# Performance work log

Hardware: AMD Instinct MI355X
Metric: run time of the kernel (lower is better)

## Reference

```python
import jax, jax.numpy as jnp
import numpy as np

DIM = 2048
STATE = 16
BATCH = 2
SEQ = 2048
LN_EPS = 1e-5


def setup_inputs() -> dict:
    key = jax.random.key(0)
    ks = jax.random.split(key, 12)
    d, n = DIM, STATE
    inp = {
        "x": jax.random.normal(ks[0], (BATCH, SEQ, d), dtype=jnp.float32),
        "ln_gamma": jnp.ones((d,), dtype=jnp.float32),
        "ln_beta": jnp.zeros((d,), dtype=jnp.float32),
        # proj_in: Linear(d, 2d) (spectral-normed; weights treated as effective)
        "W_in": jax.random.normal(ks[1], (2 * d, d), dtype=jnp.float32) / np.sqrt(d),
        "b_in": jnp.zeros((2 * d,), dtype=jnp.float32),
        "state_A": jax.random.normal(ks[2], (n, d), dtype=jnp.float32) * 0.01,
        "W_B": jax.random.normal(ks[3], (n, d), dtype=jnp.float32) / np.sqrt(d),
        "b_B": jnp.zeros((n,), dtype=jnp.float32),
        "W_C": jax.random.normal(ks[4], (n, d), dtype=jnp.float32) / np.sqrt(d),
        "b_C": jnp.zeros((n,), dtype=jnp.float32),
        "W_dt": jax.random.normal(ks[5], (d, d), dtype=jnp.float32) / np.sqrt(d),
        "b_dt": jnp.zeros((d,), dtype=jnp.float32),
        "W_out": jax.random.normal(ks[6], (d, d), dtype=jnp.float32) / np.sqrt(d),
        "b_out": jnp.zeros((d,), dtype=jnp.float32),
    }
    return inp


def reference(x, ln_gamma, ln_beta, W_in, b_in, state_A, W_B, b_B, W_C, b_C,
              W_dt, b_dt, W_out, b_out):
    residual = x
    # LayerNorm over last dim
    mu = jnp.mean(x, axis=-1, keepdims=True)
    var = jnp.mean(jnp.square(x - mu), axis=-1, keepdims=True)
    xn = (x - mu) * jax.lax.rsqrt(var + LN_EPS) * ln_gamma + ln_beta
    # input projection and gate split
    xz = jnp.einsum('bsd,ed->bse', xn, W_in) + b_in          # (B,S,2D)
    x_ssm, z = jnp.split(xz, 2, axis=-1)                      # (B,S,D) each
    # dt = clamp(softplus(proj_dt(x_ssm)), max=1.0)
    dt = jnp.minimum(jax.nn.softplus(jnp.einsum('bsd,ed->bse', x_ssm, W_dt) + b_dt), 1.0)
    Bm = jnp.einsum('bsd,nd->bsn', x_ssm, W_B) + b_B          # (B,S,N)
    Cm = jnp.einsum('bsd,nd->bsn', x_ssm, W_C) + b_C          # (B,S,N)
    # A_bar[b,s,n,d] = exp(state_A[n,d] * dt[b,s,d])
    A_bar = jnp.exp(state_A[None, None, :, :] * dt[:, :, None, :])  # (B,S,N,D)
    # y[b,s,d] = sum_n C[b,s,n]*B[b,s,n]*A_bar[b,s,n,d] * x_ssm[b,s,d]
    y = jnp.einsum('bsn,bsnd->bsd', Cm * Bm, A_bar) * x_ssm
    gated = y * jax.nn.silu(z)
    out = jnp.einsum('bsd,ed->bse', gated, W_out) + b_out
    return out + residual
```

## Files before the change

kernel.cpp:

```cpp
#include <hip/hip_runtime.h>

typedef unsigned short u16;
typedef float f32x4 __attribute__((ext_vector_type(4)));
typedef __bf16 bf16x8 __attribute__((ext_vector_type(8)));

__device__ __forceinline__ u16 f2bf(float f) {
    unsigned u = __float_as_uint(f);
    u += 0x7FFFu + ((u >> 16) & 1u);
    return (u16)(u >> 16);
}
__device__ __forceinline__ float b2f(u16 h) {
    return __uint_as_float(((unsigned)h) << 16);
}

__device__ __forceinline__ void async16(const u16* g, u16* l) {
    __builtin_amdgcn_global_load_lds(
        (__attribute__((address_space(1))) void*)(u16*)g,
        (__attribute__((address_space(3))) void*)l,
        16, 0, 0);
}

#define T_TOK 4096
#define DIM   2048

__global__ __launch_bounds__(256) void castln_all(const float* __restrict__ W_in,
                                                  u16* __restrict__ wb_in,
                                                  const float* __restrict__ W_dt,
                                                  u16* __restrict__ wb_dt,
                                                  const float* __restrict__ W_B,
                                                  const float* __restrict__ W_C,
                                                  const float* __restrict__ W_out,
                                                  u16* __restrict__ wb_out,
                                                  const float* __restrict__ x,
                                                  const float* __restrict__ g,
                                                  const float* __restrict__ b,
                                                  u16* __restrict__ o) {
    __shared__ float s1[4], s2[4];
    int blk = blockIdx.x, tid = threadIdx.x;
    if (blk < 16448) {
        const float* s; u16* d; int j;
        if (blk < 8192)       { s = W_in;  d = wb_in;  j = blk * 256 + tid; }
        else if (blk < 12288) { s = W_dt;  d = wb_dt;  j = (blk - 8192) * 256 + tid; }
        else if (blk < 12320) { s = W_B;   d = wb_dt + (size_t)2048 * 2048;
                                j = (blk - 12288) * 256 + tid; }
        else if (blk < 12352) { s = W_C;   d = wb_dt + (size_t)2064 * 2048;
                                j = (blk - 12320) * 256 + tid; }
        else                  { s = W_out; d = wb_out; j = (blk - 12352) * 256 + tid; }
        float4 f = ((const float4*)s)[j];
        ushort4 u;
        u.x = f2bf(f.x); u.y = f2bf(f.y); u.z = f2bf(f.z); u.w = f2bf(f.w);
        ((ushort4*)d)[j] = u;
        return;
    }
    int t = blk - 16448;
    int wave = tid >> 6, lane = tid & 63;
    size_t base = (size_t)t * DIM;
    int d0 = tid * 8;
    float4 v0 = *(const float4*)(x + base + d0);
    float4 v1 = *(const float4*)(x + base + d0 + 4);
    float v[8] = {v0.x, v0.y, v0.z, v0.w, v1.x, v1.y, v1.z, v1.w};
    float s = 0.f;
#pragma unroll
    for (int j = 0; j < 8; ++j) s += v[j];
#pragma unroll
    for (int o2 = 32; o2; o2 >>= 1) s += __shfl_xor(s, o2);
    if (lane == 0) s1[wave] = s;
    __syncthreads();
    float mu = (s1[0] + s1[1] + s1[2] + s1[3]) * (1.f / DIM);
    float q = 0.f;
#pragma unroll
    for (int j = 0; j < 8; ++j) { float dd = v[j] - mu; q += dd * dd; }
#pragma unroll
    for (int o2 = 32; o2; o2 >>= 1) q += __shfl_xor(q, o2);
    if (lane == 0) s2[wave] = q;
    __syncthreads();
    float var = (s2[0] + s2[1] + s2[2] + s2[3]) * (1.f / DIM);
    float rs = rsqrtf(var + 1e-5f);
    float4 g0 = *(const float4*)(g + d0), g1 = *(const float4*)(g + d0 + 4);
    float4 b0 = *(const float4*)(b + d0), b1 = *(const float4*)(b + d0 + 4);
    float gv[8] = {g0.x, g0.y, g0.z, g0.w, g1.x, g1.y, g1.z, g1.w};
    float bv[8] = {b0.x, b0.y, b0.z, b0.w, b1.x, b1.y, b1.z, b1.w};
    ushort4 r0, r1;
    u16* rp0 = (u16*)&r0; u16* rp1 = (u16*)&r1;
#pragma unroll
    for (int j = 0; j < 4; ++j) {
        rp0[j] = f2bf((v[j] - mu) * rs * gv[j] + bv[j]);
        rp1[j] = f2bf((v[j + 4] - mu) * rs * gv[j + 4] + bv[j + 4]);
    }
    *(ushort4*)(o + base + d0) = r0;
    *(ushort4*)(o + base + d0 + 4) = r1;
}

#define GBM 256
#define GBN 256
#define GBK 64

#define WAITV2 asm volatile("s_waitcnt vmcnt(2)" ::: "memory")

__global__ __launch_bounds__(512) void gemm_wide(const u16* __restrict__ A,
                                                 const u16* __restrict__ W,
                                                 const float* __restrict__ bias,
                                                 u16* __restrict__ Xs,
                                                 u16* __restrict__ Z, int K) {
    __shared__ __align__(16) u16 lA[2][GBM * GBK];
    __shared__ __align__(16) u16 lB[2][GBN * GBK];
    const int tid = threadIdx.x;
    const int wv = tid >> 6, lane = tid & 63;
    const int quad = lane >> 4, l16 = lane & 15;
    const int wr = wv >> 2, wc = wv & 3;
    const int tM = blockIdx.x * GBM, tN = blockIdx.y * GBN;

    const int srow = tid >> 3;
    const int swz = ((tid & 7) ^ (srow & 7)) * 8;
    const u16* gA = A + (size_t)(tM + srow) * 2048 + swz;
    const u16* gW = W + (size_t)(tN + srow) * 2048 + swz;

#define STAGE_AH(BI, KC, H) do {                                              \
    _Pragma("unroll") for (int r_ = 2 * (H); r_ < 2 * (H) + 2; ++r_)          \
      async16(gA + (size_t)r_ * 64 * 2048 + (KC),                             \
              &lA[BI][(r_ * 64 + wv * 8) * GBK]);                             \
  } while (0)
#define STAGE_BH(BI, KC, H) do {                                              \
    _Pragma("unroll") for (int r_ = 2 * (H); r_ < 2 * (H) + 2; ++r_)          \
      async16(gW + (size_t)r_ * 64 * 2048 + (KC),                             \
              &lB[BI][(r_ * 64 + wv * 8) * GBK]);                             \
  } while (0)

    int aoff[2][4][2], boff[2][2][2];
#pragma unroll
    for (int qm = 0; qm < 2; ++qm)
#pragma unroll
        for (int mi = 0; mi < 4; ++mi)
#pragma unroll
            for (int h = 0; h < 2; ++h) {
                int row = wr * 128 + (qm * 4 + mi) * 16 + l16;
                aoff[qm][mi][h] = row * GBK + (((h * 4 + quad) ^ (l16 & 7)) * 8);
            }
#pragma unroll
    for (int qn = 0; qn < 2; ++qn)
#pragma unroll
        for (int ni = 0; ni < 2; ++ni)
#pragma unroll
            for (int h = 0; h < 2; ++h) {
                int row = wc * 64 + (qn * 2 + ni) * 16 + l16;
                boff[qn][ni][h] = row * GBK + (((h * 4 + quad) ^ (l16 & 7)) * 8);
            }

    f32x4 acc[8][4] = {};
    bf16x8 af[4][2];

#define PHASE(BI, QM, QN, LOADA, STAGE_STMT, WAIT_STMT) do {                  \
    if (LOADA) {                                                              \
      _Pragma("unroll") for (int mi_ = 0; mi_ < 4; ++mi_)                     \
        _Pragma("unroll") for (int h_ = 0; h_ < 2; ++h_)                      \
          af[mi_][h_] = *(const bf16x8*)&lA[BI][aoff[QM][mi_][h_]];           \
    }                                                                         \
    bf16x8 bfr_[2][2];                                                        \
    _Pragma("unroll") for (int ni_ = 0; ni_ < 2; ++ni_)                       \
      _Pragma("unroll") for (int h_ = 0; h_ < 2; ++h_)                        \
        bfr_[ni_][h_] = *(const bf16x8*)&lB[BI][boff[QN][ni_][h_]];           \
    STAGE_STMT;                                                               \
    __builtin_amdgcn_s_setprio(1);                                            \
    _Pragma("unroll") for (int mi_ = 0; mi_ < 4; ++mi_)                       \
      _Pragma("unroll") for (int ni_ = 0; ni_ < 2; ++ni_)                     \
        _Pragma("unroll") for (int h_ = 0; h_ < 2; ++h_)                      \
          acc[QM * 4 + mi_][QN * 2 + ni_] =                                   \
              __builtin_amdgcn_mfma_f32_16x16x32_bf16(                        \
                  af[mi_][h_], bfr_[ni_][h_],                                 \
                  acc[QM * 4 + mi_][QN * 2 + ni_], 0, 0, 0);                  \
    __builtin_amdgcn_s_setprio(0);                                            \
    WAIT_STMT;                                                                \
    __builtin_amdgcn_s_barrier();                                             \
  } while (0)

    STAGE_AH(0, 0, 0);
    STAGE_AH(0, 0, 1);
    STAGE_BH(0, 0, 0);
    STAGE_BH(0, 0, 1);
    STAGE_AH(1, 64, 0);
    WAITV2;
    __builtin_amdgcn_s_barrier();

    const int NIT = K >> 7;
    for (int it = 0; it < NIT; ++it) {
        const int k1 = it * 128 + 64;
        int kn = it * 128 + 128;
        if (kn > K - 64) kn = K - 64;
        int kn1 = it * 128 + 192;
        if (kn1 > K - 64) kn1 = K - 64;

        PHASE(0, 0, 0, 1, STAGE_AH(1, k1, 1),  (void)0);
        PHASE(0, 0, 1, 0, STAGE_BH(1, k1, 0),  (void)0);
        PHASE(0, 1, 0, 1, STAGE_BH(1, k1, 1),  (void)0);
        PHASE(0, 1, 1, 0, STAGE_AH(0, kn, 0),  WAITV2);
        PHASE(1, 0, 0, 1, STAGE_AH(0, kn, 1),  (void)0);
        PHASE(1, 0, 1, 0, STAGE_BH(0, kn, 0),  (void)0);
        PHASE(1, 1, 0, 1, STAGE_BH(0, kn, 1),  (void)0);
        PHASE(1, 1, 1, 0, STAGE_AH(1, kn1, 0), WAITV2);
    }

    asm volatile("s_waitcnt vmcnt(0)" ::: "memory");

    const bool isb_z = (tN >= 2048);
    u16* dst = isb_z ? Z : Xs;
#pragma unroll
    for (int mi = 0; mi < 8; ++mi) {
#pragma unroll
        for (int ni = 0; ni < 4; ++ni) {
            int col = tN + wc * 64 + ni * 16 + l16;
            float bv = bias[col];
            int ocol = isb_z ? (col - 2048) : col;
#pragma unroll
            for (int r = 0; r < 4; ++r) {
                int row = tM + wr * 128 + mi * 16 + quad * 4 + r;
                dst[(size_t)row * 2048 + ocol] = f2bf(acc[mi][ni][r] + bv);
            }
        }
    }
#undef PHASE
#undef STAGE_AH
#undef STAGE_BH
}

#define DBM 128
#define DBN 128
#define DBK 64

template <int EPI>
__global__ __launch_bounds__(256) void gemm128(const u16* __restrict__ A,
                                               const u16* __restrict__ W,
                                               const float* __restrict__ bias,
                                               const float* __restrict__ resid,
                                               void* __restrict__ C,
                                               u16* __restrict__ dots, int K) {
    __shared__ __align__(16) u16 lAB[(DBM + DBN) * DBK];
    const int tid = threadIdx.x;
    const int wave = tid >> 6, lane = tid & 63;
    const int quad = lane >> 4, l16 = lane & 15;
    const int tM = blockIdx.x * DBM;
    const int tN = blockIdx.y * DBN;
    const int wr = wave >> 1, wc = wave & 1;

    const int rowin = tid >> 3;
    const int col8 = ((tid & 7) ^ (rowin & 7)) * 8;
    const u16* gptr[8];
    u16* ldst[8];
#pragma unroll
    for (int i = 0; i < 8; ++i) {
        int trow = i * 32 + rowin;
        const u16* src = (i < 4) ? (A + (size_t)(tM + trow) * 2048)
                                 : (W + (size_t)(tN + (trow - DBM)) * 2048);
        gptr[i] = src + col8;
        ldst[i] = &lAB[(i * 32 + wave * 8) * DBK];
    }

    int a_off[2][4], b_off[2][4];
#pragma unroll
    for (int h = 0; h < 2; ++h) {
#pragma unroll
        for (int mi = 0; mi < 4; ++mi)
            a_off[h][mi] = (wr * 64 + mi * 16 + l16) * DBK +
                           (((h * 4 + quad) ^ (l16 & 7)) * 8);
#pragma unroll
        for (int ni = 0; ni < 4; ++ni)
            b_off[h][ni] = (DBM + wc * 64 + ni * 16 + l16) * DBK +
                           (((h * 4 + quad) ^ (l16 & 7)) * 8);
    }

    f32x4 acc[4][4] = {};

    for (int kt = 0; kt < K; kt += DBK) {
#pragma unroll
        for (int i = 0; i < 8; ++i) async16(gptr[i] + kt, ldst[i]);
        __syncthreads();
#pragma unroll
        for (int h = 0; h < 2; ++h) {
            bf16x8 af[4], bfr[4];
#pragma unroll
            for (int i = 0; i < 4; ++i) af[i] = *(const bf16x8*)&lAB[a_off[h][i]];
#pragma unroll
            for (int i = 0; i < 4; ++i) bfr[i] = *(const bf16x8*)&lAB[b_off[h][i]];
#pragma unroll
            for (int mi = 0; mi < 4; ++mi)
#pragma unroll
                for (int ni = 0; ni < 4; ++ni)
                    acc[mi][ni] = __builtin_amdgcn_mfma_f32_16x16x32_bf16(
                        af[mi], bfr[ni], acc[mi][ni], 0, 0, 0);
        }
        __syncthreads();
    }

#pragma unroll
    for (int mi = 0; mi < 4; ++mi) {
#pragma unroll
        for (int ni = 0; ni < 4; ++ni) {
            int col = tN + wc * 64 + ni * 16 + l16;
#pragma unroll
            for (int r = 0; r < 4; ++r) {
                int row = tM + wr * 64 + mi * 16 + quad * 4 + r;
                if constexpr (EPI == 1) {
                    if (col < 2048) {
                        float v = acc[mi][ni][r] + bias[col];
                        float sp = (v > 0.5413f) ? 1.0f
                                                 : __logf(1.0f + __expf(v));
                        ((u16*)C)[(size_t)row * 2048 + col] = f2bf(sp);
                    } else if (col < 2080) {
                        dots[(size_t)row * 32 + (col - 2048)] =
                            f2bf(acc[mi][ni][r]);
                    }
                } else {
                    size_t idx = (size_t)row * 2048 + col;
                    ((float*)C)[idx] = acc[mi][ni][r] + bias[col] + resid[idx];
                }
            }
        }
    }
}

__global__ __launch_bounds__(256) void ssm_gate2_kernel(const u16* __restrict__ dtb,
                                                        const u16* __restrict__ xsb,
                                                        u16* __restrict__ zg,
                                                        const float* __restrict__ A,
                                                        const u16* __restrict__ dots,
                                                        const float* __restrict__ bB,
                                                        const float* __restrict__ bC) {
    __shared__ float Pl[8][16];
    const int tid = threadIdx.x;
    const int t0 = blockIdx.x * 8;
    const int d0 = tid * 8;

    float a[16][8];
#pragma unroll
    for (int n = 0; n < 16; ++n) {
        float4 a0 = *(const float4*)(A + n * DIM + d0);
        float4 a1 = *(const float4*)(A + n * DIM + d0 + 4);
        a[n][0] = a0.x; a[n][1] = a0.y; a[n][2] = a0.z; a[n][3] = a0.w;
        a[n][4] = a1.x; a[n][5] = a1.y; a[n][6] = a1.z; a[n][7] = a1.w;
    }
    if (tid < 128) {
        int tt = tid >> 4, n = tid & 15;
        float Bv = b2f(dots[(size_t)(t0 + tt) * 32 + n]) + bB[n];
        float Cv = b2f(dots[(size_t)(t0 + tt) * 32 + 16 + n]) + bC[n];
        Pl[tt][n] = Bv * Cv;
    }
    __syncthreads();

    for (int tt = 0; tt < 8; ++tt) {
        size_t dbase = (size_t)(t0 + tt) * DIM;
        ushort4 dth0 = *(const ushort4*)(dtb + dbase + d0);
        ushort4 dth1 = *(const ushort4*)(dtb + dbase + d0 + 4);
        ushort4 xsh0 = *(const ushort4*)(xsb + dbase + d0);
        ushort4 xsh1 = *(const ushort4*)(xsb + dbase + d0 + 4);
        ushort4 zh0  = *(const ushort4*)(zg + dbase + d0);
        ushort4 zh1  = *(const ushort4*)(zg + dbase + d0 + 4);
        float dtv[8], xsv[8], zv[8];
        const u16* dp0 = (const u16*)&dth0; const u16* dp1 = (const u16*)&dth1;
        const u16* xp0 = (const u16*)&xsh0; const u16* xp1 = (const u16*)&xsh1;
        const u16* zp0 = (const u16*)&zh0;  const u16* zp1 = (const u16*)&zh1;
#pragma unroll
        for (int j = 0; j < 4; ++j) {
            dtv[j] = b2f(dp0[j]); dtv[j + 4] = b2f(dp1[j]);
            xsv[j] = b2f(xp0[j]); xsv[j + 4] = b2f(xp1[j]);
            zv[j]  = b2f(zp0[j]); zv[j + 4]  = b2f(zp1[j]);
        }
        float s[8] = {};
#pragma unroll
        for (int n = 0; n < 16; ++n) {
            float pn = Pl[tt][n];
#pragma unroll
            for (int j = 0; j < 8; ++j) s[j] += pn * __expf(a[n][j] * dtv[j]);
        }
        ushort4 r0, r1;
        u16* rp0 = (u16*)&r0; u16* rp1 = (u16*)&r1;
#pragma unroll
        for (int j = 0; j < 8; ++j) {
            float y = s[j] * xsv[j];
            float sz = zv[j] * (1.0f / (1.0f + __expf(-zv[j])));
            u16 hv = f2bf(y * sz);
            if (j < 4) rp0[j] = hv; else rp1[j - 4] = hv;
        }
        *(ushort4*)(zg + dbase + d0) = r0;
        *(ushort4*)(zg + dbase + d0 + 4) = r1;
    }
}

extern "C" void kernel_launch(void* const* d_in, const int* in_sizes, int n_in,
                              void* d_out, int out_size, void* d_ws, size_t ws_size,
                              hipStream_t stream) {
    const float* x      = (const float*)d_in[0];
    const float* ln_g   = (const float*)d_in[1];
    const float* ln_b   = (const float*)d_in[2];
    const float* W_in   = (const float*)d_in[3];
    const float* b_in   = (const float*)d_in[4];
    const float* stateA = (const float*)d_in[5];
    const float* W_B    = (const float*)d_in[6];
    const float* b_B    = (const float*)d_in[7];
    const float* W_C    = (const float*)d_in[8];
    const float* b_C    = (const float*)d_in[9];
    const float* W_dt   = (const float*)d_in[10];
    const float* b_dt   = (const float*)d_in[11];
    const float* W_out  = (const float*)d_in[12];
    const float* b_out  = (const float*)d_in[13];

    char* ws = (char*)d_ws;
    u16*   wb_in  = (u16*)(ws);
    u16*   dotsb  = (u16*)(ws);
    u16*   xnb    = (u16*)(ws + 16777216);
    u16*   dtb    = (u16*)(ws + 16777216);
    u16*   xsb    = (u16*)(ws + 33554432);
    u16*   zg     = (u16*)(ws + 50331648);
    u16*   wb_dt  = (u16*)(ws + 67108864);
    u16*   wb_out = (u16*)(ws + 75759616);

    castln_all<<<20544, 256, 0, stream>>>(W_in, wb_in, W_dt, wb_dt, W_B, W_C,
                                          W_out, wb_out, x, ln_g, ln_b, xnb);
    gemm_wide<<<dim3(16, 16), 512, 0, stream>>>(xnb, wb_in, b_in, xsb, zg, 2048);
    gemm128<1><<<dim3(32, 17), 256, 0, stream>>>(xsb, wb_dt, b_dt, nullptr,
                                                 dtb, dotsb, 2048);
    ssm_gate2_kernel<<<512, 256, 0, stream>>>(dtb, xsb, zg, stateA, dotsb,
                                              b_B, b_C);
    gemm128<2><<<dim3(32, 16), 256, 0, stream>>>(zg, wb_out, b_out, x,
                                                 (float*)d_out, nullptr, 2048);
}
```

Measured before the change: 396.0 us.

## Double-buffer LDS in narrow-tile GEMMs for dt and output projections

Replaces the 128x128 single-buffered GEMM with a 128x64 tile that keeps two LDS buffers, issuing async loads for the next K-step while MFMAs run on the current one. This drops one barrier per iteration. The narrower tile doubles the grid (about 1056 and 1024 blocks) to fill more CUs on the 4096x2048 problems. The trade-off is lower arithmetic intensity per tile and more total global traffic for the A operand.

```diff
diff --git a/kernel.cpp b/kernel.cpp
--- a/kernel.cpp
+++ b/kernel.cpp
@@ -222,95 +222,107 @@
 #undef STAGE_BH
 }
 
-#define DBM 128
-#define DBN 128
-#define DBK 64
+#define NBM 128
+#define NBN 64
+#define NBK 64
 
 template <int EPI>
-__global__ __launch_bounds__(256) void gemm128(const u16* __restrict__ A,
-                                               const u16* __restrict__ W,
+__global__ __launch_bounds__(256) void gemm_nw(const u16* __restrict__ A, int lda,
+                                               const u16* __restrict__ W, int ldw,
                                                const float* __restrict__ bias,
                                                const float* __restrict__ resid,
-                                               void* __restrict__ C,
-                                               u16* __restrict__ dots, int K) {
-    __shared__ __align__(16) u16 lAB[(DBM + DBN) * DBK];
+                                               void* __restrict__ C, int ldc, int K,
+                                               u16* __restrict__ dots) {
+    __shared__ __align__(16) u16 lAB[2][(NBM + NBN) * NBK];
     const int tid = threadIdx.x;
     const int wave = tid >> 6, lane = tid & 63;
     const int quad = lane >> 4, l16 = lane & 15;
-    const int tM = blockIdx.x * DBM;
-    const int tN = blockIdx.y * DBN;
+    const int tM = blockIdx.x * NBM;
+    const int tN = blockIdx.y * NBN;
     const int wr = wave >> 1, wc = wave & 1;
 
     const int rowin = tid >> 3;
     const int col8 = ((tid & 7) ^ (rowin & 7)) * 8;
-    const u16* gptr[8];
-    u16* ldst[8];
-#pragma unroll
-    for (int i = 0; i < 8; ++i) {
+    const u16* gptr[6];
+    int loff[6];
+#pragma unroll
+    for (int i = 0; i < 6; ++i) {
         int trow = i * 32 + rowin;
-        const u16* src = (i < 4) ? (A + (size_t)(tM + trow) * 2048)
-                                 : (W + (size_t)(tN + (trow - DBM)) * 2048);
+        const u16* src = (i < 4) ? (A + (size_t)(tM + trow) * lda)
+                                 : (W + (size_t)(tN + (trow - NBM)) * ldw);
         gptr[i] = src + col8;
-        ldst[i] = &lAB[(i * 32 + wave * 8) * DBK];
-    }
-
-    int a_off[2][4], b_off[2][4];
+        loff[i] = (i * 32 + wave * 8) * NBK;
+    }
+
+    int a_off[2][4], b_off[2][2];
 #pragma unroll
     for (int h = 0; h < 2; ++h) {
 #pragma unroll
         for (int mi = 0; mi < 4; ++mi)
-            a_off[h][mi] = (wr * 64 + mi * 16 + l16) * DBK +
+            a_off[h][mi] = (wr * 64 + mi * 16 + l16) * NBK +
                            (((h * 4 + quad) ^ (l16 & 7)) * 8);
 #pragma unroll
-        for (int ni = 0; ni < 4; ++ni)
-            b_off[h][ni] = (DBM + wc * 64 + ni * 16 + l16) * DBK +
+        for (int ni = 0; ni < 2; ++ni)
+            b_off[h][ni] = (NBM + wc * 32 + ni * 16 + l16) * NBK +
                            (((h * 4 + quad) ^ (l16 & 7)) * 8);
     }
 
-    f32x4 acc[4][4] = {};
-
-    for (int kt = 0; kt < K; kt += DBK) {
-#pragma unroll
-        for (int i = 0; i < 8; ++i) async16(gptr[i] + kt, ldst[i]);
+    f32x4 acc[4][2] = {};
+
+#define STAGE_NW(BUF, KT) do {                                                \
+    _Pragma("unroll") for (int i_ = 0; i_ < 6; ++i_)                          \
+      async16(gptr[i_] + (KT), &lAB[BUF][loff[i_]]);                          \
+  } while (0)
+
+    STAGE_NW(0, 0);
+    __syncthreads();
+
+    int cur = 0;
+    for (int kt = 0; kt < K; kt += NBK) {
+        if (kt + NBK < K) STAGE_NW(cur ^ 1, kt + NBK);
+        const u16* Lb = lAB[cur];
+        bf16x8 af[2][4], bfr[2][2];
+#pragma unroll
+        for (int h = 0; h < 2; ++h) {
+#pragma unroll
+            for (int mi = 0; mi < 4; ++mi) af[h][mi] = *(const bf16x8*)&Lb[a_off[h][mi]];
+#pragma unroll
+            for (int ni = 0; ni < 2; ++ni) bfr[h][ni] = *(const bf16x8*)&Lb[b_off[h][ni]];
+        }
+#pragma unroll
+        for (int h = 0; h < 2; ++h)
+#pragma unroll
+            for (int mi = 0; mi < 4; ++mi)
+#pragma unroll
+                for (int ni = 0; ni < 2; ++ni)
+                    acc[mi][ni] = __builtin_amdgcn_mfma_f32_16x16x32_bf16(
+                        af[h][mi], bfr[h][ni], acc[mi][ni], 0, 0, 0);
         __syncthreads();
-#pragma unroll
-        for (int h = 0; h < 2; ++h) {
-            bf16x8 af[4], bfr[4];
-#pragma unroll
-            for (int i = 0; i < 4; ++i) af[i] = *(const bf16x8*)&lAB[a_off[h][i]];
-#pragma unroll
-            for (int i = 0; i < 4; ++i) bfr[i] = *(const bf16x8*)&lAB[b_off[h][i]];
-#pragma unroll
-            for (int mi = 0; mi < 4; ++mi)
-#pragma unroll
-                for (int ni = 0; ni < 4; ++ni)
-                    acc[mi][ni] = __builtin_amdgcn_mfma_f32_16x16x32_bf16(
-                        af[mi], bfr[ni], acc[mi][ni], 0, 0, 0);
-        }
-        __syncthreads();
-    }
+        cur ^= 1;
+    }
+#undef STAGE_NW
 
 #pragma unroll
     for (int mi = 0; mi < 4; ++mi) {
 #pragma unroll
-        for (int ni = 0; ni < 4; ++ni) {
-            int col = tN + wc * 64 + ni * 16 + l16;
+        for (int ni = 0; ni < 2; ++ni) {
+            int col = tN + wc * 32 + ni * 16 + l16;
+            float bv = (EPI == 1 && col >= 2048) ? 0.f : bias[col];
 #pragma unroll
             for (int r = 0; r < 4; ++r) {
                 int row = tM + wr * 64 + mi * 16 + quad * 4 + r;
+                float v = acc[mi][ni][r] + bv;
                 if constexpr (EPI == 1) {
                     if (col < 2048) {
-                        float v = acc[mi][ni][r] + bias[col];
                         float sp = (v > 0.5413f) ? 1.0f
                                                  : __logf(1.0f + __expf(v));
-                        ((u16*)C)[(size_t)row * 2048 + col] = f2bf(sp);
+                        ((u16*)C)[(size_t)row * ldc + col] = f2bf(sp);
                     } else if (col < 2080) {
-                        dots[(size_t)row * 32 + (col - 2048)] =
-                            f2bf(acc[mi][ni][r]);
+                        dots[(size_t)row * 32 + (col - 2048)] = f2bf(v);
                     }
                 } else {
-                    size_t idx = (size_t)row * 2048 + col;
-                    ((float*)C)[idx] = acc[mi][ni][r] + bias[col] + resid[idx];
+                    size_t idx = (size_t)row * ldc + col;
+                    ((float*)C)[idx] = v + resid[idx];
                 }
             }
         }
@@ -415,10 +427,10 @@
     castln_all<<<20544, 256, 0, stream>>>(W_in, wb_in, W_dt, wb_dt, W_B, W_C,
                                           W_out, wb_out, x, ln_g, ln_b, xnb);
     gemm_wide<<<dim3(16, 16), 512, 0, stream>>>(xnb, wb_in, b_in, xsb, zg, 2048);
-    gemm128<1><<<dim3(32, 17), 256, 0, stream>>>(xsb, wb_dt, b_dt, nullptr,
-                                                 dtb, dotsb, 2048);
+    gemm_nw<1><<<dim3(32, 33), 256, 0, stream>>>(xsb, 2048, wb_dt, 2048, b_dt,
+                                                 nullptr, dtb, 2048, 2048, dotsb);
     ssm_gate2_kernel<<<512, 256, 0, stream>>>(dtb, xsb, zg, stateA, dotsb,
                                               b_B, b_C);
-    gemm128<2><<<dim3(32, 16), 256, 0, stream>>>(zg, wb_out, b_out, x,
-                                                 (float*)d_out, nullptr, 2048);
-}
+    gemm_nw<2><<<dim3(32, 32), 256, 0, stream>>>(zg, 2048, wb_out, 2048, b_out,
+                                                 x, (float*)d_out, 2048, 2048, nullptr);
+}
```

Result: faster. 360.6 us (-8.9%).
